# Optimization experiments

Measured on AMD Instinct MI355X. Metric: run time of the kernel, lower is better.

The kernel has to match this reference:

```python
import jax, jax.numpy as jnp
import numpy as np
from jax import lax


def _fuse_proj(proj):
    # proj: [B,2,4,4] -> [B,4,4]; K @ [R|t] into top 3x4 of extrinsics
    p = proj[:, 0]
    new34 = jnp.einsum('bij,bjk->bik', proj[:, 1, :3, :3], proj[:, 0, :3, :4])
    return p.at[:, :3, :4].set(new34)


def _homo_warp(src_fea, src_proj, ref_proj, depth_values):
    # src_fea [B,C,H,W], src_proj/ref_proj [B,4,4], depth_values [B,D]
    B, C, H, W = src_fea.shape
    D = depth_values.shape[1]
    proj = jnp.einsum('bij,bjk->bik', src_proj, jnp.linalg.inv(ref_proj))
    rot, trans = proj[:, :3, :3], proj[:, :3, 3:4]
    y, x = jnp.meshgrid(jnp.arange(H, dtype=src_fea.dtype),
                        jnp.arange(W, dtype=src_fea.dtype), indexing='ij')
    xyz = jnp.stack([x.ravel(), y.ravel(), jnp.ones(H * W, src_fea.dtype)])  # [3,HW]
    rot_xyz = jnp.einsum('bij,jk->bik', rot, xyz)                            # [B,3,HW]
    pxyz = rot_xyz[:, :, None, :] * depth_values[:, None, :, None] + trans[:, :, None, :]  # [B,3,D,HW]
    z = pxyz[:, 2]
    px = pxyz[:, 0] / z   # pixel coords (align_corners=True convention)
    py = pxyz[:, 1] / z
    # bilinear sample with zeros padding
    x0 = jnp.floor(px); y0 = jnp.floor(py)
    x1 = x0 + 1.0;      y1 = y0 + 1.0
    wx1 = px - x0; wx0 = 1.0 - wx1
    wy1 = py - y0; wy0 = 1.0 - wy1
    fea_flat = src_fea.reshape(B, C, H * W)

    def corner(xc, yc, w):
        valid = (xc >= 0) & (xc <= W - 1) & (yc >= 0) & (yc <= H - 1)
        idx = (jnp.clip(yc, 0, H - 1).astype(jnp.int32) * W
               + jnp.clip(xc, 0, W - 1).astype(jnp.int32)).reshape(B, -1)   # [B,D*HW]
        g = jax.vmap(lambda f, i: jnp.take(f, i, axis=1))(fea_flat, idx)    # [B,C,D*HW]
        return g * (w * valid.astype(w.dtype)).reshape(B, 1, -1)

    out = (corner(x0, y0, wx0 * wy0) + corner(x1, y0, wx1 * wy0)
           + corner(x0, y1, wx0 * wy1) + corner(x1, y1, wx1 * wy1))
    return out.reshape(B, C, D, H, W)


def _forward(features, proj_matrices, depth_values, reg_w, num_depth):
    N = features.shape[0]
    ref_fea = features[0]                      # [B,C,H,W]
    ref_proj = _fuse_proj(proj_matrices[:, 0])
    B, C, H, W = ref_fea.shape
    D = num_depth

    vol_sum = jnp.broadcast_to(ref_fea[:, :, None], (B, C, D, H, W))
    vol_sq = vol_sum ** 2
    for i in range(1, N):                      # small fixed view loop
        src_proj = _fuse_proj(proj_matrices[:, i])
        wv = _homo_warp(features[i], src_proj, ref_proj, depth_values)
        vol_sum = vol_sum + wv
        vol_sq = vol_sq + wv ** 2
    inv_n = 1.0 / N
    variance = vol_sq * inv_n - (vol_sum * inv_n) ** 2   # [B,C,D,H,W]

    # cost regularization: 3x3x3 conv C->1 (stand-in for external 3D CNN)
    cost = lax.conv_general_dilated(variance, reg_w, (1, 1, 1), 'SAME',
                                    dimension_numbers=('NCDHW', 'OIDHW', 'NCDHW'))[:, 0]  # [B,D,H,W]
    prob = jax.nn.softmax(cost, axis=1)
    depth = jnp.sum(prob * depth_values[:, :, None, None], axis=1)          # [B,H,W]

    # photometric confidence (no-grad block)
    p = lax.stop_gradient(prob)
    # 4*avg_pool3d(pad(prob,(1,2)) over depth, kernel (4,1,1)) == sliding sum of 4
    sum4 = lax.reduce_window(p, 0.0, lax.add, (1, 4, 1, 1), (1, 1, 1, 1),
                             ((0, 0), (1, 2), (0, 0), (0, 0)))
    didx = jnp.sum(p * jnp.arange(D, dtype=p.dtype)[None, :, None, None], axis=1)
    didx = jnp.clip(didx.astype(jnp.int32), 0, D - 1)                        # [B,H,W]
    conf = jnp.take_along_axis(sum4, didx[:, None], axis=1)[:, 0]            # [B,H,W]
    return depth, conf


def setup_inputs() -> dict:
    key = jax.random.key(0)
    k1, k2, k3 = jax.random.split(key, 3)
    N, B, C, H, W, D = 5, 1, 32, 128, 160, 48
    features = jax.random.normal(k1, (N, B, C, H, W), jnp.float32)
    eye = jnp.eye(4, dtype=jnp.float32)
    proj_matrices = eye + 0.01 * jax.random.normal(k2, (B, N, 2, 4, 4), jnp.float32)
    depth_values = jnp.broadcast_to(
        425.0 + 510.0 * jnp.arange(D, dtype=jnp.float32) / (D - 1), (B, D))
    reg_w = 0.05 * jax.random.normal(k3, (1, C, 3, 3, 3), jnp.float32)
    return {"features": features, "proj_matrices": proj_matrices,
            "depth_values": depth_values, "reg_w": reg_w, "num_depth": D}


def reference(features, proj_matrices, depth_values, reg_w, num_depth):
    return _forward(features, proj_matrices, depth_values, reg_w, num_depth)
```

## Files before the change

### kernel.cpp

```cpp
#include <hip/hip_runtime.h>

#define W_ 160
#define H_ 128
#define C_ 32
#define D_ 48
#define HW_ (H_*W_)
#define TX 16
#define TY 16
#define HPX 18
#define HPY 18
#define NHP (HPX*HPY)
#define NHPP 336
#define NT 21
#define DSTW 29

typedef _Float16 h8 __attribute__((ext_vector_type(8)));
typedef __fp16 fp16x2 __attribute__((ext_vector_type(2)));
typedef float f4 __attribute__((ext_vector_type(4)));

__device__ __forceinline__ _Float16 u2h(unsigned int u) {
    union { unsigned short s; _Float16 h; } x; x.s = (unsigned short)u; return x.h;
}
__device__ __forceinline__ unsigned int pkh2(float a, float b) {
    union { fp16x2 h; unsigned int u; } x;
    x.h = __builtin_amdgcn_cvt_pkrtz(a, b);
    return x.u;
}

__device__ __forceinline__ void inv4x4(const float* a, float* inv) {
    inv[0]  =  a[5]*a[10]*a[15] - a[5]*a[11]*a[14] - a[9]*a[6]*a[15] + a[9]*a[7]*a[14] + a[13]*a[6]*a[11] - a[13]*a[7]*a[10];
    inv[4]  = -a[4]*a[10]*a[15] + a[4]*a[11]*a[14] + a[8]*a[6]*a[15] - a[8]*a[7]*a[14] - a[12]*a[6]*a[11] + a[12]*a[7]*a[10];
    inv[8]  =  a[4]*a[9]*a[15]  - a[4]*a[11]*a[13] - a[8]*a[5]*a[15] + a[8]*a[7]*a[13] + a[12]*a[5]*a[11] - a[12]*a[7]*a[9];
    inv[12] = -a[4]*a[9]*a[14]  + a[4]*a[10]*a[13] + a[8]*a[5]*a[14] - a[8]*a[6]*a[13] - a[12]*a[5]*a[10] + a[12]*a[6]*a[9];
    inv[1]  = -a[1]*a[10]*a[15] + a[1]*a[11]*a[14] + a[9]*a[2]*a[15] - a[9]*a[3]*a[14] - a[13]*a[2]*a[11] + a[13]*a[3]*a[10];
    inv[5]  =  a[0]*a[10]*a[15] - a[0]*a[11]*a[14] - a[8]*a[2]*a[15] + a[8]*a[3]*a[14] + a[12]*a[2]*a[11] - a[12]*a[3]*a[10];
    inv[9]  = -a[0]*a[9]*a[15]  + a[0]*a[11]*a[13] + a[8]*a[1]*a[15] - a[8]*a[3]*a[13] - a[12]*a[1]*a[11] + a[12]*a[3]*a[9];
    inv[13] =  a[0]*a[9]*a[14]  - a[0]*a[10]*a[13] - a[8]*a[1]*a[14] + a[8]*a[2]*a[13] + a[12]*a[1]*a[10] - a[12]*a[2]*a[9];
    inv[2]  =  a[1]*a[6]*a[15]  - a[1]*a[7]*a[14]  - a[5]*a[2]*a[15] + a[5]*a[3]*a[14] + a[13]*a[2]*a[7]  - a[13]*a[3]*a[6];
    inv[6]  = -a[0]*a[6]*a[15]  + a[0]*a[7]*a[14]  + a[4]*a[2]*a[15] - a[4]*a[3]*a[14] - a[12]*a[2]*a[7]  + a[12]*a[3]*a[6];
    inv[10] =  a[0]*a[5]*a[15]  - a[0]*a[7]*a[13]  - a[4]*a[1]*a[15] + a[4]*a[3]*a[13] + a[12]*a[1]*a[7]  - a[12]*a[3]*a[5];
    inv[14] = -a[0]*a[5]*a[14]  + a[0]*a[6]*a[13]  + a[4]*a[1]*a[14] - a[4]*a[2]*a[13] - a[12]*a[1]*a[6]  + a[12]*a[2]*a[5];
    inv[3]  = -a[1]*a[6]*a[11]  + a[1]*a[7]*a[10]  + a[5]*a[2]*a[11] - a[5]*a[3]*a[10] - a[9]*a[2]*a[7]   + a[9]*a[3]*a[6];
    inv[7]  =  a[0]*a[6]*a[11]  - a[0]*a[7]*a[10]  - a[4]*a[2]*a[11] + a[4]*a[3]*a[10] + a[8]*a[2]*a[7]   - a[8]*a[3]*a[6];
    inv[11] = -a[0]*a[5]*a[11]  + a[0]*a[7]*a[9]   + a[4]*a[1]*a[11] - a[4]*a[3]*a[9]  - a[8]*a[1]*a[7]   + a[8]*a[3]*a[5];
    inv[15] =  a[0]*a[5]*a[10]  - a[0]*a[6]*a[9]   - a[4]*a[1]*a[10] + a[4]*a[2]*a[9]  + a[8]*a[1]*a[6]   - a[8]*a[2]*a[5];
    float det = a[0]*inv[0] + a[1]*inv[4] + a[2]*inv[8] + a[3]*inv[12];
    float id = 1.0f / det;
    for (int i = 0; i < 16; ++i) inv[i] *= id;
}

__device__ __forceinline__ void fuseProj(const float* proj, int i, float* F) {
    const float* A = proj + i*32;
    const float* R = A + 16;
    for (int r = 0; r < 3; ++r)
        for (int k = 0; k < 4; ++k)
            F[r*4+k] = R[r*4]*A[k] + R[r*4+1]*A[4+k] + R[r*4+2]*A[8+k];
    for (int k = 0; k < 4; ++k) F[12+k] = A[12+k];
}

__global__ __launch_bounds__(256) void kS(const float* __restrict__ f,
                                          const float* __restrict__ proj,
                                          _Float16* __restrict__ ft,
                                          float* __restrict__ RX,
                                          float* __restrict__ M) {
    __shared__ float t[64][33];
    const int bx = blockIdx.x, v = blockIdx.y;
    const int tid = threadIdx.x;
    if (bx < 320) {
        const int p0 = bx * 64;
        const int q = tid & 15;
        const int ch0 = tid >> 4;
        #pragma unroll
        for (int j = 0; j < 2; ++j) {
            const int ch = ch0 + j*16;
            const float4 v4 = *(const float4*)&f[(size_t)(v*C_ + ch)*HW_ + p0 + q*4];
            t[q*4 + 0][ch] = v4.x;
            t[q*4 + 1][ch] = v4.y;
            t[q*4 + 2][ch] = v4.z;
            t[q*4 + 3][ch] = v4.w;
        }
        __syncthreads();
        const int px = tid >> 2;
        const int c0 = (tid & 3) * 8;
        h8 o;
        #pragma unroll
        for (int k = 0; k < 8; ++k) o[k] = (_Float16)t[px][c0 + k];
        *(h8*)&ft[((size_t)(v*HW_ + p0 + px) << 5) + c0] = o;
    } else {
        if (v >= 4) return;
        float F0[16], Fv[16], inv[16], P[12];
        fuseProj(proj, 0, F0);
        fuseProj(proj, v + 1, Fv);
        inv4x4(F0, inv);
        #pragma unroll
        for (int r = 0; r < 3; ++r)
            #pragma unroll
            for (int c = 0; c < 4; ++c) {
                float acc = 0.f;
                #pragma unroll
                for (int k = 0; k < 4; ++k) acc += Fv[r*4+k]*inv[k*4+c];
                P[r*4+c] = acc;
            }
        const int p = (bx - 320)*256 + tid;
        const float x = (float)(p % W_), y = (float)(p / W_);
        float4 o;
        o.x = P[0]*x + P[1]*y + P[2];
        o.y = P[4]*x + P[5]*y + P[6];
        o.z = P[8]*x + P[9]*y + P[10];
        o.w = 0.f;
        ((float4*)RX)[(size_t)v*HW_ + p] = o;
        if (bx == 320 && tid == 0) {
            float* om = M + v*12;
            om[0]=P[0]; om[1]=P[1]; om[2]=P[2];
            om[3]=P[4]; om[4]=P[5]; om[5]=P[6];
            om[6]=P[8]; om[7]=P[9]; om[8]=P[10];
            om[9]=P[3]; om[10]=P[7]; om[11]=P[11];
        }
    }
}

__global__ __launch_bounds__(256) void kA(const _Float16* __restrict__ featH,
                                          const float* __restrict__ RX,
                                          const float* __restrict__ M,
                                          const float* __restrict__ dvals,
                                          const float* __restrict__ regw,
                                          float* __restrict__ Q) {
    __shared__ __align__(16) unsigned DLP[NHPP*DSTW];

    const int tid = threadIdx.x;
    const int bx = blockIdx.x, by = blockIdx.y;
    const int d0 = blockIdx.z*2, d1 = d0 + 1;
    const int lane = tid & 63;
    const int wv = tid >> 6;
    const int n = lane & 15;
    const int grp = lane >> 4;
    const float dv0 = dvals[d0], dv1 = dvals[d1];
    const float tx = M[grp*12 + 9], ty = M[grp*12 + 10], tz = M[grp*12 + 11];

    h8 bf0, bf1;
    {
        const int kb = grp * 8;
        #pragma unroll
        for (int j = 0; j < 8; ++j) {
            const int ch = kb + j;
            bf0[j] = (_Float16)regw[ch*27 + n];
            bf1[j] = (_Float16)((n < 11) ? regw[ch*27 + 16 + n] : 0.f);
        }
    }

    const h8 hz = {(_Float16)0,(_Float16)0,(_Float16)0,(_Float16)0,
                   (_Float16)0,(_Float16)0,(_Float16)0,(_Float16)0};
    const h8* F = (const h8*)featH;
    const float4* RX4 = (const float4*)RX;
    const f4 fz = {0.f, 0.f, 0.f, 0.f};

    auto mk = [&](int tile, bool& pokO, int& rpO) {
        const int px = tile*16 + n;
        const int hx = px % HPX;
        const int hy = px / HPX;
        const int lx = bx*TX + hx - 1;
        const int ly = by*TY + hy - 1;
        pokO = (px < NHP) && (lx >= 0) && (lx < W_) && (ly >= 0) && (ly < H_);
        rpO = pokO ? (ly*W_ + lx) : 0;
    };

    bool pok; int rp;
    mk(wv, pok, rp);
    float4 a = RX4[(size_t)grp*HW_ + rp];
    h8 fr = F[(size_t)rp*4 + grp];

    #pragma unroll 1
    for (int pass = 0; pass < 6; ++pass) {
        const int tile = pass*4 + wv;

        bool pokN = false; int rpN = 0;
        float4 aN = {0.f, 0.f, 0.f, 0.f};
        h8 frN = hz;
        if (pass < 5) {
            mk(tile + 4, pokN, rpN);
            aN = RX4[(size_t)grp*HW_ + rpN];
            frN = F[(size_t)rpN*4 + grp];
        }

        if (tile < NT) {
            unsigned pidx, pwax, pway, pwbx, pwby;
            {
                const float z0 = a.z*dv0 + tz;
                const float rz0 = 1.0f / z0;
                const float pxf0 = fminf(fmaxf((a.x*dv0 + tx)*rz0, -8.f), 168.f);
                const float pyf0 = fminf(fmaxf((a.y*dv0 + ty)*rz0, -8.f), 136.f);
                const float fx = floorf(pxf0), fy = floorf(pyf0);
                const float mxl = (fx >= 0.f  && fx <= 159.f) ? 1.f : 0.f;
                const float mxh = (fx >= -1.f && fx <= 158.f) ? 1.f : 0.f;
                const float myl = (fy >= 0.f  && fy <= 127.f) ? 1.f : 0.f;
                const float myh = (fy >= -1.f && fy <= 126.f) ? 1.f : 0.f;
                const int xs = (int)fminf(fmaxf(fx + 1.f, 0.f), 160.f);
                const int ys = (int)fminf(fmaxf(fy + 1.f, 0.f), 128.f);
                const int x0 = max(xs-1, 0), x1 = min(xs, W_-1);
                const int y0 = max(ys-1, 0), y1 = min(ys, H_-1);
                pidx = (unsigned)x0 | ((unsigned)x1 << 8)
                     | ((unsigned)y0 << 16) | ((unsigned)y1 << 24);
                const float wx1a = pxf0 - fx, wy1a = pyf0 - fy;
                pwax = pkh2((1.f - wx1a)*mxl, wx1a*mxh);
                pway = pkh2((1.f - wy1a)*myl, wy1a*myh);
                const float z1 = a.z*dv1 + tz;
                const float rz1 = 1.0f / z1;
                const float pxf1 = fminf(fmaxf((a.x*dv1 + tx)*rz1, -8.f), 168.f);
                const float pyf1 = fminf(fmaxf((a.y*dv1 + ty)*rz1, -8.f), 136.f);
                const float wx1b = pxf1 - fx, wy1b = pyf1 - fy;
                pwbx = pkh2((1.f - wx1b)*mxl, wx1b*mxh);
                pwby = pkh2((1.f - wy1b)*myl, wy1b*myh);
                if (!pok) { pwax = 0u; pway = 0u; pwbx = 0u; pwby = 0u; }
            }

            h8 var0 = hz, var1 = hz;
            h8 s0 = hz, q0 = hz, s1 = hz, q1 = hz;
            if (pok) {
                s0 = fr; q0 = fr*fr; s1 = fr; q1 = q0;
            }

            unsigned idxc, axc, ayc, bxc, byc;
            {
                const int src = n;
                idxc = (unsigned)__shfl((int)pidx, src, 64);
                axc  = (unsigned)__shfl((int)pwax, src, 64);
                ayc  = (unsigned)__shfl((int)pway, src, 64);
                bxc  = (unsigned)__shfl((int)pwbx, src, 64);
                byc  = (unsigned)__shfl((int)pwby, src, 64);
            }
            h8 f00 = hz, f10 = hz, f01 = hz, f11 = hz;
            if (pok) {
                const int x0 = idxc & 0xff, x1 = (idxc >> 8) & 0xff;
                const int y0W = ((idxc >> 16) & 0xff) * W_;
                const int y1W = (idxc >> 24) * W_;
                const h8* Fv = F + (size_t)1*HW_*4;
                f00 = Fv[(size_t)(y0W+x0)*4 + grp];
                f10 = Fv[(size_t)(y0W+x1)*4 + grp];
                f01 = Fv[(size_t)(y1W+x0)*4 + grp];
                f11 = Fv[(size_t)(y1W+x1)*4 + grp];
            }

            #pragma unroll
            for (int v = 0; v < 4; ++v) {
                unsigned idxn = 0u, axn = 0u, ayn = 0u, bxn = 0u, byn = 0u;
                h8 n00 = hz, n10 = hz, n01 = hz, n11 = hz;
                if (v < 3) {
                    const int src = (v+1)*16 + n;
                    idxn = (unsigned)__shfl((int)pidx, src, 64);
                    axn  = (unsigned)__shfl((int)pwax, src, 64);
                    ayn  = (unsigned)__shfl((int)pway, src, 64);
                    bxn  = (unsigned)__shfl((int)pwbx, src, 64);
                    byn  = (unsigned)__shfl((int)pwby, src, 64);
                    if (pok) {
                        const int x0 = idxn & 0xff, x1 = (idxn >> 8) & 0xff;
                        const int y0W = ((idxn >> 16) & 0xff) * W_;
                        const int y1W = (idxn >> 24) * W_;
                        const h8* Fv = F + (size_t)(v+2)*HW_*4;
                        n00 = Fv[(size_t)(y0W+x0)*4 + grp];
                        n10 = Fv[(size_t)(y0W+x1)*4 + grp];
                        n01 = Fv[(size_t)(y1W+x0)*4 + grp];
                        n11 = Fv[(size_t)(y1W+x1)*4 + grp];
                    }
                }
                if (pok) {
                    const _Float16 wx0a = u2h(axc), wx1a = u2h(axc >> 16);
                    const _Float16 wy0a = u2h(ayc), wy1a = u2h(ayc >> 16);
                    const h8 t0a = f00*wx0a + f10*wx1a;
                    const h8 t1a = f01*wx0a + f11*wx1a;
                    const h8 g0 = t0a*wy0a + t1a*wy1a;
                    s0 += g0; q0 += g0*g0;
                    const _Float16 wx0b = u2h(bxc), wx1b = u2h(bxc >> 16);
                    const _Float16 wy0b = u2h(byc), wy1b = u2h(byc >> 16);
                    const h8 t0b = f00*wx0b + f10*wx1b;
                    const h8 t1b = f01*wx0b + f11*wx1b;
                    const h8 g1 = t0b*wy0b + t1b*wy1b;
                    s1 += g1; q1 += g1*g1;
                }
                f00 = n00; f10 = n10; f01 = n01; f11 = n11;
                idxc = idxn; axc = axn; ayc = ayn; bxc = bxn; byc = byn;
            }

            if (pok) {
                const _Float16 c5 = (_Float16)0.2f;
                const h8 sa = s0 * c5, sb = s1 * c5;
                var0 = q0*c5 - sa*sa;
                var1 = q1*c5 - sb*sb;
            }
            const f4 a0 = __builtin_amdgcn_mfma_f32_16x16x32_f16(var0, bf0, fz, 0, 0, 0);
            const f4 b0 = __builtin_amdgcn_mfma_f32_16x16x32_f16(var0, bf1, fz, 0, 0, 0);
            const f4 a1 = __builtin_amdgcn_mfma_f32_16x16x32_f16(var1, bf0, fz, 0, 0, 0);
            const f4 b1 = __builtin_amdgcn_mfma_f32_16x16x32_f16(var1, bf1, fz, 0, 0, 0);
            const int rbase = tile*16 + grp*4;
            #pragma unroll
            for (int r = 0; r < 4; ++r) {
                unsigned* dr = &DLP[(rbase + r)*DSTW];
                dr[n] = pkh2(a0[r], a1[r]);
                if (n < 11) dr[16 + n] = pkh2(b0[r], b1[r]);
            }
        }

        pok = pokN; rp = rpN; a = aN; fr = frN;
    }
    __syncthreads();

    {
        const int x = tid & 15;
        const int y = tid >> 4;
        float c00 = 0.f, c01 = 0.f, c02 = 0.f;
        float c10 = 0.f, c11 = 0.f, c12 = 0.f;
        #pragma unroll
        for (int jy = 0; jy < 3; ++jy) {
            #pragma unroll
            for (int jx = 0; jx < 3; ++jx) {
                const int sp = jy*3 + jx;
                const unsigned* dr = &DLP[((y + jy)*HPX + (x + jx))*DSTW];
                const unsigned u0 = dr[sp];
                const unsigned u1 = dr[9 + sp];
                const unsigned u2 = dr[18 + sp];
                c00 += (float)u2h(u0);  c10 += (float)u2h(u0 >> 16);
                c01 += (float)u2h(u1);  c11 += (float)u2h(u1 >> 16);
                c02 += (float)u2h(u2);  c12 += (float)u2h(u2 >> 16);
            }
        }
        const int p = (by*TY + y)*W_ + bx*TX + x;
        Q[(size_t)(0*D_ + d0)*HW_ + p] = c00;
        Q[(size_t)(1*D_ + d0)*HW_ + p] = c01;
        Q[(size_t)(2*D_ + d0)*HW_ + p] = c02;
        Q[(size_t)(0*D_ + d1)*HW_ + p] = c10;
        Q[(size_t)(1*D_ + d1)*HW_ + p] = c11;
        Q[(size_t)(2*D_ + d1)*HW_ + p] = c12;
    }
}

__global__ __launch_bounds__(256) void kB(const float* __restrict__ Q,
                                          const float* __restrict__ dvals,
                                          float* __restrict__ out) {
    __shared__ float Rm[4][64], Sm[4][64], Sd[4][64], Si[4][64], Cf[4][64];
    const int tid = threadIdx.x;
    const int l = tid & 63;
    const int w = tid >> 6;
    const int p = blockIdx.x*64 + l;
    const int db = w*12;
    const float* Q0 = Q;
    const float* Q1 = Q + (size_t)D_*HW_;
    const float* Q2 = Q + (size_t)2*D_*HW_;

    float c[12];
    #pragma unroll
    for (int j = 0; j < 12; ++j) {
        const int dd = db + j;
        float v = Q1[dd*HW_ + p];
        if (dd > 0)     v += Q0[(dd-1)*HW_ + p];
        if (dd < D_-1)  v += Q2[(dd+1)*HW_ + p];
        c[j] = v;
    }
    float lm = c[0];
    #pragma unroll
    for (int j = 1; j < 12; ++j) lm = fmaxf(lm, c[j]);
    Rm[w][l] = lm;
    __syncthreads();
    const float gm = fmaxf(fmaxf(Rm[0][l], Rm[1][l]), fmaxf(Rm[2][l], Rm[3][l]));

    float e[12];
    float ls = 0.f, lsd = 0.f, lsi = 0.f;
    #pragma unroll
    for (int j = 0; j < 12; ++j) {
        const int dd = db + j;
        const float ev = __expf(c[j] - gm);
        e[j] = ev;
        ls  += ev;
        lsd += ev * dvals[dd];
        lsi += ev * (float)dd;
    }
    Sm[w][l] = ls; Sd[w][l] = lsd; Si[w][l] = lsi;
    __syncthreads();
    const float ts  = Sm[0][l] + Sm[1][l] + Sm[2][l] + Sm[3][l];
    const float tsd = Sd[0][l] + Sd[1][l] + Sd[2][l] + Sd[3][l];
    const float tsi = Si[0][l] + Si[1][l] + Si[2][l] + Si[3][l];
    const float is = 1.f / ts;
    int di = (int)(tsi * is);
    di = di < 0 ? 0 : (di > D_-1 ? D_-1 : di);

    float lc = 0.f;
    #pragma unroll
    for (int j = 0; j < 12; ++j) {
        const int dd = db + j;
        lc += ((dd >= di-1) && (dd <= di+2)) ? e[j] : 0.f;
    }
    Cf[w][l] = lc;
    __syncthreads();
    if (w == 0) {
        out[p] = tsd * is;
        out[HW_ + p] = (Cf[0][l] + Cf[1][l] + Cf[2][l] + Cf[3][l]) * is;
    }
}

extern "C" void kernel_launch(void* const* d_in, const int* in_sizes, int n_in,
                              void* d_out, int out_size, void* d_ws, size_t ws_size,
                              hipStream_t stream) {
    const float* features = (const float*)d_in[0];
    const float* proj     = (const float*)d_in[1];
    const float* dvals    = (const float*)d_in[2];
    const float* regw     = (const float*)d_in[3];
    float* out = (float*)d_out;

    _Float16* featH = (_Float16*)d_ws;
    float* RX = (float*)(featH + (size_t)5*HW_*C_);
    float* M  = RX + (size_t)4*HW_*4;
    float* Q  = M + 64;

    kS<<<dim3(400, 5), 256, 0, stream>>>(features, proj, featH, RX, M);
    kA<<<dim3(W_/TX, H_/TY, D_/2), 256, 0, stream>>>(featH, RX, M, dvals, regw, Q);
    kB<<<HW_/64, 256, 0, stream>>>(Q, dvals, out);
}
```

Measured before the change: 133.0 us.

## Recompute rotated pixel rays in kA and issue gathers for all views earlier

Drops the precomputed per-pixel rotated-coordinate buffer RX. kA now loads the 3x3 rotation from M and recomputes the ray for each halo pixel with a few FMAs, and kS shrinks to one matrix-setup block per view. This removes a global write and a re-read of a float4 per pixel per view. The gather loop is also restructured so the shuffles and four-corner loads for several views are in flight before accumulation, which raises memory-level parallelism at the cost of more registers.

Result: no change. 134.4 us (+1.1%).

```diff
diff --git a/kernel.cpp b/kernel.cpp
--- a/kernel.cpp
+++ b/kernel.cpp
@@ -61,7 +61,6 @@
 __global__ __launch_bounds__(256) void kS(const float* __restrict__ f,
                                           const float* __restrict__ proj,
                                           _Float16* __restrict__ ft,
-                                          float* __restrict__ RX,
                                           float* __restrict__ M) {
     __shared__ float t[64][33];
     const int bx = blockIdx.x, v = blockIdx.y;
@@ -87,7 +86,7 @@
         for (int k = 0; k < 8; ++k) o[k] = (_Float16)t[px][c0 + k];
         *(h8*)&ft[((size_t)(v*HW_ + p0 + px) << 5) + c0] = o;
     } else {
-        if (v >= 4) return;
+        if (v >= 4 || tid != 0) return;
         float F0[16], Fv[16], inv[16], P[12];
         fuseProj(proj, 0, F0);
         fuseProj(proj, v + 1, Fv);
@@ -101,26 +100,15 @@
                 for (int k = 0; k < 4; ++k) acc += Fv[r*4+k]*inv[k*4+c];
                 P[r*4+c] = acc;
             }
-        const int p = (bx - 320)*256 + tid;
-        const float x = (float)(p % W_), y = (float)(p / W_);
-        float4 o;
-        o.x = P[0]*x + P[1]*y + P[2];
-        o.y = P[4]*x + P[5]*y + P[6];
-        o.z = P[8]*x + P[9]*y + P[10];
-        o.w = 0.f;
-        ((float4*)RX)[(size_t)v*HW_ + p] = o;
-        if (bx == 320 && tid == 0) {
-            float* om = M + v*12;
-            om[0]=P[0]; om[1]=P[1]; om[2]=P[2];
-            om[3]=P[4]; om[4]=P[5]; om[5]=P[6];
-            om[6]=P[8]; om[7]=P[9]; om[8]=P[10];
-            om[9]=P[3]; om[10]=P[7]; om[11]=P[11];
-        }
+        float* om = M + v*12;
+        om[0]=P[0]; om[1]=P[1]; om[2]=P[2];
+        om[3]=P[4]; om[4]=P[5]; om[5]=P[6];
+        om[6]=P[8]; om[7]=P[9]; om[8]=P[10];
+        om[9]=P[3]; om[10]=P[7]; om[11]=P[11];
     }
 }
 
 __global__ __launch_bounds__(256) void kA(const _Float16* __restrict__ featH,
-                                          const float* __restrict__ RX,
                                           const float* __restrict__ M,
                                           const float* __restrict__ dvals,
                                           const float* __restrict__ regw,
@@ -135,7 +123,11 @@
     const int n = lane & 15;
     const int grp = lane >> 4;
     const float dv0 = dvals[d0], dv1 = dvals[d1];
-    const float tx = M[grp*12 + 9], ty = M[grp*12 + 10], tz = M[grp*12 + 11];
+    const float* Mg = M + grp*12;
+    const float P0 = Mg[0], P1 = Mg[1], P2 = Mg[2];
+    const float P3 = Mg[3], P4 = Mg[4], P5 = Mg[5];
+    const float P6 = Mg[6], P7 = Mg[7], P8 = Mg[8];
+    const float tx = Mg[9], ty = Mg[10], tz = Mg[11];
 
     h8 bf0, bf1;
     {
@@ -151,44 +143,44 @@
     const h8 hz = {(_Float16)0,(_Float16)0,(_Float16)0,(_Float16)0,
                    (_Float16)0,(_Float16)0,(_Float16)0,(_Float16)0};
     const h8* F = (const h8*)featH;
-    const float4* RX4 = (const float4*)RX;
     const f4 fz = {0.f, 0.f, 0.f, 0.f};
 
-    auto mk = [&](int tile, bool& pokO, int& rpO) {
+    auto mk = [&](int tile, bool& pokO, int& rpO, int& lxO, int& lyO) {
         const int px = tile*16 + n;
         const int hx = px % HPX;
         const int hy = px / HPX;
-        const int lx = bx*TX + hx - 1;
-        const int ly = by*TY + hy - 1;
-        pokO = (px < NHP) && (lx >= 0) && (lx < W_) && (ly >= 0) && (ly < H_);
-        rpO = pokO ? (ly*W_ + lx) : 0;
+        lxO = bx*TX + hx - 1;
+        lyO = by*TY + hy - 1;
+        pokO = (px < NHP) && (lxO >= 0) && (lxO < W_) && (lyO >= 0) && (lyO < H_);
+        rpO = pokO ? (lyO*W_ + lxO) : 0;
     };
 
-    bool pok; int rp;
-    mk(wv, pok, rp);
-    float4 a = RX4[(size_t)grp*HW_ + rp];
+    bool pok; int rp, lx, ly;
+    mk(wv, pok, rp, lx, ly);
     h8 fr = F[(size_t)rp*4 + grp];
 
     #pragma unroll 1
     for (int pass = 0; pass < 6; ++pass) {
         const int tile = pass*4 + wv;
 
-        bool pokN = false; int rpN = 0;
-        float4 aN = {0.f, 0.f, 0.f, 0.f};
+        bool pokN = false; int rpN = 0, lxN = 0, lyN = 0;
         h8 frN = hz;
         if (pass < 5) {
-            mk(tile + 4, pokN, rpN);
-            aN = RX4[(size_t)grp*HW_ + rpN];
+            mk(tile + 4, pokN, rpN, lxN, lyN);
             frN = F[(size_t)rpN*4 + grp];
         }
 
         if (tile < NT) {
             unsigned pidx, pwax, pway, pwbx, pwby;
             {
-                const float z0 = a.z*dv0 + tz;
+                const float xf = (float)lx, yf = (float)ly;
+                const float rx = fmaf(P0, xf, fmaf(P1, yf, P2));
+                const float ry = fmaf(P3, xf, fmaf(P4, yf, P5));
+                const float rz = fmaf(P6, xf, fmaf(P7, yf, P8));
+                const float z0 = rz*dv0 + tz;
                 const float rz0 = 1.0f / z0;
-                const float pxf0 = fminf(fmaxf((a.x*dv0 + tx)*rz0, -8.f), 168.f);
-                const float pyf0 = fminf(fmaxf((a.y*dv0 + ty)*rz0, -8.f), 136.f);
+                const float pxf0 = fminf(fmaxf((rx*dv0 + tx)*rz0, -8.f), 168.f);
+                const float pyf0 = fminf(fmaxf((ry*dv0 + ty)*rz0, -8.f), 136.f);
                 const float fx = floorf(pxf0), fy = floorf(pyf0);
                 const float mxl = (fx >= 0.f  && fx <= 159.f) ? 1.f : 0.f;
                 const float mxh = (fx >= -1.f && fx <= 158.f) ? 1.f : 0.f;
@@ -203,83 +195,72 @@
                 const float wx1a = pxf0 - fx, wy1a = pyf0 - fy;
                 pwax = pkh2((1.f - wx1a)*mxl, wx1a*mxh);
                 pway = pkh2((1.f - wy1a)*myl, wy1a*myh);
-                const float z1 = a.z*dv1 + tz;
+                const float z1 = rz*dv1 + tz;
                 const float rz1 = 1.0f / z1;
-                const float pxf1 = fminf(fmaxf((a.x*dv1 + tx)*rz1, -8.f), 168.f);
-                const float pyf1 = fminf(fmaxf((a.y*dv1 + ty)*rz1, -8.f), 136.f);
+                const float pxf1 = fminf(fmaxf((rx*dv1 + tx)*rz1, -8.f), 168.f);
+                const float pyf1 = fminf(fmaxf((ry*dv1 + ty)*rz1, -8.f), 136.f);
                 const float wx1b = pxf1 - fx, wy1b = pyf1 - fy;
                 pwbx = pkh2((1.f - wx1b)*mxl, wx1b*mxh);
                 pwby = pkh2((1.f - wy1b)*myl, wy1b*myh);
                 if (!pok) { pwax = 0u; pway = 0u; pwbx = 0u; pwby = 0u; }
             }
 
-            h8 var0 = hz, var1 = hz;
             h8 s0 = hz, q0 = hz, s1 = hz, q1 = hz;
-            if (pok) {
-                s0 = fr; q0 = fr*fr; s1 = fr; q1 = q0;
-            }
-
-            unsigned idxc, axc, ayc, bxc, byc;
-            {
-                const int src = n;
-                idxc = (unsigned)__shfl((int)pidx, src, 64);
-                axc  = (unsigned)__shfl((int)pwax, src, 64);
-                ayc  = (unsigned)__shfl((int)pway, src, 64);
-                bxc  = (unsigned)__shfl((int)pwbx, src, 64);
-                byc  = (unsigned)__shfl((int)pwby, src, 64);
-            }
-            h8 f00 = hz, f10 = hz, f01 = hz, f11 = hz;
-            if (pok) {
-                const int x0 = idxc & 0xff, x1 = (idxc >> 8) & 0xff;
-                const int y0W = ((idxc >> 16) & 0xff) * W_;
-                const int y1W = (idxc >> 24) * W_;
-                const h8* Fv = F + (size_t)1*HW_*4;
-                f00 = Fv[(size_t)(y0W+x0)*4 + grp];
-                f10 = Fv[(size_t)(y0W+x1)*4 + grp];
-                f01 = Fv[(size_t)(y1W+x0)*4 + grp];
-                f11 = Fv[(size_t)(y1W+x1)*4 + grp];
-            }
-
-            #pragma unroll
-            for (int v = 0; v < 4; ++v) {
-                unsigned idxn = 0u, axn = 0u, ayn = 0u, bxn = 0u, byn = 0u;
-                h8 n00 = hz, n10 = hz, n01 = hz, n11 = hz;
-                if (v < 3) {
-                    const int src = (v+1)*16 + n;
-                    idxn = (unsigned)__shfl((int)pidx, src, 64);
-                    axn  = (unsigned)__shfl((int)pwax, src, 64);
-                    ayn  = (unsigned)__shfl((int)pway, src, 64);
-                    bxn  = (unsigned)__shfl((int)pwbx, src, 64);
-                    byn  = (unsigned)__shfl((int)pwby, src, 64);
-                    if (pok) {
-                        const int x0 = idxn & 0xff, x1 = (idxn >> 8) & 0xff;
-                        const int y0W = ((idxn >> 16) & 0xff) * W_;
-                        const int y1W = (idxn >> 24) * W_;
-                        const h8* Fv = F + (size_t)(v+2)*HW_*4;
-                        n00 = Fv[(size_t)(y0W+x0)*4 + grp];
-                        n10 = Fv[(size_t)(y0W+x1)*4 + grp];
-                        n01 = Fv[(size_t)(y1W+x0)*4 + grp];
-                        n11 = Fv[(size_t)(y1W+x1)*4 + grp];
-                    }
-                }
+            if (pok) { s0 = fr; q0 = fr*fr; s1 = fr; q1 = q0; }
+
+            auto SH = [&](int v, unsigned& i, unsigned& wax, unsigned& way,
+                          unsigned& wbx, unsigned& wby) {
+                const int src = v*16 + n;
+                i   = (unsigned)__shfl((int)pidx, src, 64);
+                wax = (unsigned)__shfl((int)pwax, src, 64);
+                way = (unsigned)__shfl((int)pway, src, 64);
+                wbx = (unsigned)__shfl((int)pwbx, src, 64);
+                wby = (unsigned)__shfl((int)pwby, src, 64);
+            };
+            auto LD = [&](int v, unsigned i, h8& c00, h8& c10, h8& c01, h8& c11) {
                 if (pok) {
-                    const _Float16 wx0a = u2h(axc), wx1a = u2h(axc >> 16);
-                    const _Float16 wy0a = u2h(ayc), wy1a = u2h(ayc >> 16);
-                    const h8 t0a = f00*wx0a + f10*wx1a;
-                    const h8 t1a = f01*wx0a + f11*wx1a;
+                    const int x0 = i & 0xff, x1 = (i >> 8) & 0xff;
+                    const int y0W = ((i >> 16) & 0xff) * W_;
+                    const int y1W = (i >> 24) * W_;
+                    const h8* Fv = F + (size_t)(v+1)*HW_*4;
+                    c00 = Fv[(size_t)(y0W+x0)*4 + grp];
+                    c10 = Fv[(size_t)(y0W+x1)*4 + grp];
+                    c01 = Fv[(size_t)(y1W+x0)*4 + grp];
+                    c11 = Fv[(size_t)(y1W+x1)*4 + grp];
+                } else { c00 = hz; c10 = hz; c01 = hz; c11 = hz; }
+            };
+            auto ACC = [&](unsigned wax, unsigned way, unsigned wbx, unsigned wby,
+                           h8 c00, h8 c10, h8 c01, h8 c11) {
+                if (pok) {
+                    const _Float16 wx0a = u2h(wax), wx1a = u2h(wax >> 16);
+                    const _Float16 wy0a = u2h(way), wy1a = u2h(way >> 16);
+                    const h8 t0a = c00*wx0a + c10*wx1a;
+                    const h8 t1a = c01*wx0a + c11*wx1a;
                     const h8 g0 = t0a*wy0a + t1a*wy1a;
                     s0 += g0; q0 += g0*g0;
-                    const _Float16 wx0b = u2h(bxc), wx1b = u2h(bxc >> 16);
-                    const _Float16 wy0b = u2h(byc), wy1b = u2h(byc >> 16);
-                    const h8 t0b = f00*wx0b + f10*wx1b;
-                    const h8 t1b = f01*wx0b + f11*wx1b;
+                    const _Float16 wx0b = u2h(wbx), wx1b = u2h(wbx >> 16);
+                    const _Float16 wy0b = u2h(wby), wy1b = u2h(wby >> 16);
+                    const h8 t0b = c00*wx0b + c10*wx1b;
+                    const h8 t1b = c01*wx0b + c11*wx1b;
                     const h8 g1 = t0b*wy0b + t1b*wy1b;
                     s1 += g1; q1 += g1*g1;
                 }
-                f00 = n00; f10 = n10; f01 = n01; f11 = n11;
-                idxc = idxn; axc = axn; ayc = ayn; bxc = bxn; byc = byn;
-            }
-
+            };
+
+            unsigned i0,ax0,ay0,bx0,by0; SH(0,i0,ax0,ay0,bx0,by0);
+            unsigned i1,ax1,ay1,bx1,by1; SH(1,i1,ax1,ay1,bx1,by1);
+            h8 A00,A10,A01,A11; LD(0,i0,A00,A10,A01,A11);
+            h8 B00,B10,B01,B11; LD(1,i1,B00,B10,B01,B11);
+            unsigned i2,ax2,ay2,bx2,by2; SH(2,i2,ax2,ay2,bx2,by2);
+            h8 C00,C10,C01,C11; LD(2,i2,C00,C10,C01,C11);
+            ACC(ax0,ay0,bx0,by0, A00,A10,A01,A11);
+            unsigned i3,ax3,ay3,bx3,by3; SH(3,i3,ax3,ay3,bx3,by3);
+            h8 E00,E10,E01,E11; LD(3,i3,E00,E10,E01,E11);
+            ACC(ax1,ay1,bx1,by1, B00,B10,B01,B11);
+            ACC(ax2,ay2,bx2,by2, C00,C10,C01,C11);
+            ACC(ax3,ay3,bx3,by3, E00,E10,E01,E11);
+
+            h8 var0 = hz, var1 = hz;
             if (pok) {
                 const _Float16 c5 = (_Float16)0.2f;
                 const h8 sa = s0 * c5, sb = s1 * c5;
@@ -299,7 +280,7 @@
             }
         }
 
-        pok = pokN; rp = rpN; a = aN; fr = frN;
+        pok = pokN; rp = rpN; lx = lxN; ly = lyN; fr = frN;
     }
     __syncthreads();
 
@@ -405,11 +386,10 @@
     float* out = (float*)d_out;
 
     _Float16* featH = (_Float16*)d_ws;
-    float* RX = (float*)(featH + (size_t)5*HW_*C_);
-    float* M  = RX + (size_t)4*HW_*4;
+    float* M  = (float*)(featH + (size_t)5*HW_*C_);
     float* Q  = M + 64;
 
-    kS<<<dim3(400, 5), 256, 0, stream>>>(features, proj, featH, RX, M);
-    kA<<<dim3(W_/TX, H_/TY, D_/2), 256, 0, stream>>>(featH, RX, M, dvals, regw, Q);
+    kS<<<dim3(321, 5), 256, 0, stream>>>(features, proj, featH, M);
+    kA<<<dim3(W_/TX, H_/TY, D_/2), 256, 0, stream>>>(featH, M, dvals, regw, Q);
     kB<<<HW_/64, 256, 0, stream>>>(Q, dvals, out);
 }
```

## Recompute rotated pixel rays in-kernel and use 512-thread blocks for cost volume

Applied to the files above, without the earlier changes.

Drops the precomputed per-pixel rotated-ray buffer RX: kS now writes only the 12 projection coefficients, and kA recomputes rot*[x,y,1] from the pixel coordinates with three FMAs per point. This removes a 4x HW float4 global write plus the matching reads. kA also doubles its block to 512 threads (8 waves, 3 passes instead of 6), and the final 3x3 reduction is split so each half of the block handles one of the two depths. Costs are a few extra ALU ops per point and higher per-block register pressure under the 512-thread launch bound.

Result: no change. 131.9 us (-0.8%).

```diff
diff --git a/kernel.cpp b/kernel.cpp
--- a/kernel.cpp
+++ b/kernel.cpp
@@ -61,7 +61,6 @@
 __global__ __launch_bounds__(256) void kS(const float* __restrict__ f,
                                           const float* __restrict__ proj,
                                           _Float16* __restrict__ ft,
-                                          float* __restrict__ RX,
                                           float* __restrict__ M) {
     __shared__ float t[64][33];
     const int bx = blockIdx.x, v = blockIdx.y;
@@ -87,7 +86,7 @@
         for (int k = 0; k < 8; ++k) o[k] = (_Float16)t[px][c0 + k];
         *(h8*)&ft[((size_t)(v*HW_ + p0 + px) << 5) + c0] = o;
     } else {
-        if (v >= 4) return;
+        if (v >= 4 || tid != 0) return;
         float F0[16], Fv[16], inv[16], P[12];
         fuseProj(proj, 0, F0);
         fuseProj(proj, v + 1, Fv);
@@ -101,26 +100,15 @@
                 for (int k = 0; k < 4; ++k) acc += Fv[r*4+k]*inv[k*4+c];
                 P[r*4+c] = acc;
             }
-        const int p = (bx - 320)*256 + tid;
-        const float x = (float)(p % W_), y = (float)(p / W_);
-        float4 o;
-        o.x = P[0]*x + P[1]*y + P[2];
-        o.y = P[4]*x + P[5]*y + P[6];
-        o.z = P[8]*x + P[9]*y + P[10];
-        o.w = 0.f;
-        ((float4*)RX)[(size_t)v*HW_ + p] = o;
-        if (bx == 320 && tid == 0) {
-            float* om = M + v*12;
-            om[0]=P[0]; om[1]=P[1]; om[2]=P[2];
-            om[3]=P[4]; om[4]=P[5]; om[5]=P[6];
-            om[6]=P[8]; om[7]=P[9]; om[8]=P[10];
-            om[9]=P[3]; om[10]=P[7]; om[11]=P[11];
-        }
-    }
-}
-
-__global__ __launch_bounds__(256) void kA(const _Float16* __restrict__ featH,
-                                          const float* __restrict__ RX,
+        float* om = M + v*12;
+        om[0]=P[0]; om[1]=P[1]; om[2]=P[2];
+        om[3]=P[4]; om[4]=P[5]; om[5]=P[6];
+        om[6]=P[8]; om[7]=P[9]; om[8]=P[10];
+        om[9]=P[3]; om[10]=P[7]; om[11]=P[11];
+    }
+}
+
+__global__ __launch_bounds__(512) void kA(const _Float16* __restrict__ featH,
                                           const float* __restrict__ M,
                                           const float* __restrict__ dvals,
                                           const float* __restrict__ regw,
@@ -135,7 +123,11 @@
     const int n = lane & 15;
     const int grp = lane >> 4;
     const float dv0 = dvals[d0], dv1 = dvals[d1];
-    const float tx = M[grp*12 + 9], ty = M[grp*12 + 10], tz = M[grp*12 + 11];
+    const float* Mg = M + grp*12;
+    const float P0 = Mg[0], P1 = Mg[1], P2 = Mg[2];
+    const float P3 = Mg[3], P4 = Mg[4], P5 = Mg[5];
+    const float P6 = Mg[6], P7 = Mg[7], P8 = Mg[8];
+    const float tx = Mg[9], ty = Mg[10], tz = Mg[11];
 
     h8 bf0, bf1;
     {
@@ -151,44 +143,44 @@
     const h8 hz = {(_Float16)0,(_Float16)0,(_Float16)0,(_Float16)0,
                    (_Float16)0,(_Float16)0,(_Float16)0,(_Float16)0};
     const h8* F = (const h8*)featH;
-    const float4* RX4 = (const float4*)RX;
     const f4 fz = {0.f, 0.f, 0.f, 0.f};
 
-    auto mk = [&](int tile, bool& pokO, int& rpO) {
+    auto mk = [&](int tile, bool& pokO, int& rpO, int& lxO, int& lyO) {
         const int px = tile*16 + n;
         const int hx = px % HPX;
         const int hy = px / HPX;
-        const int lx = bx*TX + hx - 1;
-        const int ly = by*TY + hy - 1;
-        pokO = (px < NHP) && (lx >= 0) && (lx < W_) && (ly >= 0) && (ly < H_);
-        rpO = pokO ? (ly*W_ + lx) : 0;
+        lxO = bx*TX + hx - 1;
+        lyO = by*TY + hy - 1;
+        pokO = (px < NHP) && (lxO >= 0) && (lxO < W_) && (lyO >= 0) && (lyO < H_);
+        rpO = pokO ? (lyO*W_ + lxO) : 0;
     };
 
-    bool pok; int rp;
-    mk(wv, pok, rp);
-    float4 a = RX4[(size_t)grp*HW_ + rp];
+    bool pok; int rp, lx, ly;
+    mk(wv, pok, rp, lx, ly);
     h8 fr = F[(size_t)rp*4 + grp];
 
     #pragma unroll 1
-    for (int pass = 0; pass < 6; ++pass) {
-        const int tile = pass*4 + wv;
-
-        bool pokN = false; int rpN = 0;
-        float4 aN = {0.f, 0.f, 0.f, 0.f};
+    for (int pass = 0; pass < 3; ++pass) {
+        const int tile = pass*8 + wv;
+
+        bool pokN = false; int rpN = 0, lxN = 0, lyN = 0;
         h8 frN = hz;
-        if (pass < 5) {
-            mk(tile + 4, pokN, rpN);
-            aN = RX4[(size_t)grp*HW_ + rpN];
+        if (pass < 2) {
+            mk(tile + 8, pokN, rpN, lxN, lyN);
             frN = F[(size_t)rpN*4 + grp];
         }
 
         if (tile < NT) {
             unsigned pidx, pwax, pway, pwbx, pwby;
             {
-                const float z0 = a.z*dv0 + tz;
+                const float xf = (float)lx, yf = (float)ly;
+                const float rx = fmaf(P0, xf, fmaf(P1, yf, P2));
+                const float ry = fmaf(P3, xf, fmaf(P4, yf, P5));
+                const float rz = fmaf(P6, xf, fmaf(P7, yf, P8));
+                const float z0 = rz*dv0 + tz;
                 const float rz0 = 1.0f / z0;
-                const float pxf0 = fminf(fmaxf((a.x*dv0 + tx)*rz0, -8.f), 168.f);
-                const float pyf0 = fminf(fmaxf((a.y*dv0 + ty)*rz0, -8.f), 136.f);
+                const float pxf0 = fminf(fmaxf((rx*dv0 + tx)*rz0, -8.f), 168.f);
+                const float pyf0 = fminf(fmaxf((ry*dv0 + ty)*rz0, -8.f), 136.f);
                 const float fx = floorf(pxf0), fy = floorf(pyf0);
                 const float mxl = (fx >= 0.f  && fx <= 159.f) ? 1.f : 0.f;
                 const float mxh = (fx >= -1.f && fx <= 158.f) ? 1.f : 0.f;
@@ -203,10 +195,10 @@
                 const float wx1a = pxf0 - fx, wy1a = pyf0 - fy;
                 pwax = pkh2((1.f - wx1a)*mxl, wx1a*mxh);
                 pway = pkh2((1.f - wy1a)*myl, wy1a*myh);
-                const float z1 = a.z*dv1 + tz;
+                const float z1 = rz*dv1 + tz;
                 const float rz1 = 1.0f / z1;
-                const float pxf1 = fminf(fmaxf((a.x*dv1 + tx)*rz1, -8.f), 168.f);
-                const float pyf1 = fminf(fmaxf((a.y*dv1 + ty)*rz1, -8.f), 136.f);
+                const float pxf1 = fminf(fmaxf((rx*dv1 + tx)*rz1, -8.f), 168.f);
+                const float pyf1 = fminf(fmaxf((ry*dv1 + ty)*rz1, -8.f), 136.f);
                 const float wx1b = pxf1 - fx, wy1b = pyf1 - fy;
                 pwbx = pkh2((1.f - wx1b)*mxl, wx1b*mxh);
                 pwby = pkh2((1.f - wy1b)*myl, wy1b*myh);
@@ -299,36 +291,33 @@
             }
         }
 
-        pok = pokN; rp = rpN; a = aN; fr = frN;
+        pok = pokN; rp = rpN; lx = lxN; ly = lyN; fr = frN;
     }
     __syncthreads();
 
     {
-        const int x = tid & 15;
-        const int y = tid >> 4;
-        float c00 = 0.f, c01 = 0.f, c02 = 0.f;
-        float c10 = 0.f, c11 = 0.f, c12 = 0.f;
+        const int half = tid >> 8;
+        const int sh = half * 16;
+        const int t2 = tid & 255;
+        const int x = t2 & 15;
+        const int y = t2 >> 4;
+        float c0 = 0.f, c1 = 0.f, c2 = 0.f;
         #pragma unroll
         for (int jy = 0; jy < 3; ++jy) {
             #pragma unroll
             for (int jx = 0; jx < 3; ++jx) {
                 const int sp = jy*3 + jx;
                 const unsigned* dr = &DLP[((y + jy)*HPX + (x + jx))*DSTW];
-                const unsigned u0 = dr[sp];
-                const unsigned u1 = dr[9 + sp];
-                const unsigned u2 = dr[18 + sp];
-                c00 += (float)u2h(u0);  c10 += (float)u2h(u0 >> 16);
-                c01 += (float)u2h(u1);  c11 += (float)u2h(u1 >> 16);
-                c02 += (float)u2h(u2);  c12 += (float)u2h(u2 >> 16);
+                c0 += (float)u2h(dr[sp] >> sh);
+                c1 += (float)u2h(dr[9 + sp] >> sh);
+                c2 += (float)u2h(dr[18 + sp] >> sh);
             }
         }
         const int p = (by*TY + y)*W_ + bx*TX + x;
-        Q[(size_t)(0*D_ + d0)*HW_ + p] = c00;
-        Q[(size_t)(1*D_ + d0)*HW_ + p] = c01;
-        Q[(size_t)(2*D_ + d0)*HW_ + p] = c02;
-        Q[(size_t)(0*D_ + d1)*HW_ + p] = c10;
-        Q[(size_t)(1*D_ + d1)*HW_ + p] = c11;
-        Q[(size_t)(2*D_ + d1)*HW_ + p] = c12;
+        const int dd = d0 + half;
+        Q[(size_t)(0*D_ + dd)*HW_ + p] = c0;
+        Q[(size_t)(1*D_ + dd)*HW_ + p] = c1;
+        Q[(size_t)(2*D_ + dd)*HW_ + p] = c2;
     }
 }
 
@@ -405,11 +394,10 @@
     float* out = (float*)d_out;
 
     _Float16* featH = (_Float16*)d_ws;
-    float* RX = (float*)(featH + (size_t)5*HW_*C_);
-    float* M  = RX + (size_t)4*HW_*4;
+    float* M  = (float*)(featH + (size_t)5*HW_*C_);
     float* Q  = M + 64;
 
-    kS<<<dim3(400, 5), 256, 0, stream>>>(features, proj, featH, RX, M);
-    kA<<<dim3(W_/TX, H_/TY, D_/2), 256, 0, stream>>>(featH, RX, M, dvals, regw, Q);
+    kS<<<dim3(321, 5), 256, 0, stream>>>(features, proj, featH, M);
+    kA<<<dim3(W_/TX, H_/TY, D_/2), 512, 0, stream>>>(featH, M, dvals, regw, Q);
     kB<<<HW_/64, 256, 0, stream>>>(Q, dvals, out);
 }
```
